# Kernel optimization log

Hardware: AMD Instinct MI355X
Metric: run time of the kernel (lower is better)

The kernel has to match this reference:

```python
import jax, jax.numpy as jnp
import numpy as np

G, P, PO, TAU = 4, 32, 128, 2.0  # n_groups, spatial_points, out_points=P*out_multiplier, level-softmax temperature
STRIDES = (4.0, 8.0, 16.0, 32.0)
EPS = 1e-5

def _ln2(x):
    # LayerNorm over last two dims, no affine (F.layer_norm(x, x.shape[-2:]))
    mu = jnp.mean(x, axis=(-2, -1), keepdims=True)
    var = jnp.var(x, axis=(-2, -1), keepdims=True)
    return (x - mu) * jax.lax.rsqrt(var + EPS)

def _ln1(x, g, b):
    mu = jnp.mean(x, axis=-1, keepdims=True)
    var = jnp.var(x, axis=-1, keepdims=True)
    return (x - mu) * jax.lax.rsqrt(var + EPS) * g + b

def _bilinear(feat, xp, yp):
    # feat: (B,G,H,W,Ce); xp,yp: (B,N,G,P) pixel coords; grid_sample bilinear,
    # zero padding, align_corners=False semantics.
    B, Gg, H, W, Ce = feat.shape
    x0 = jnp.floor(xp); y0 = jnp.floor(yp)
    wx1 = xp - x0; wy1 = yp - y0
    b_idx = jnp.arange(B)[:, None, None, None]
    g_idx = jnp.arange(Gg)[None, None, :, None]
    def gather(xi, yi):
        valid = (xi >= 0) & (xi < W) & (yi >= 0) & (yi < H)
        xc = jnp.clip(xi, 0, W - 1).astype(jnp.int32)
        yc = jnp.clip(yi, 0, H - 1).astype(jnp.int32)
        return feat[b_idx, g_idx, yc, xc] * valid[..., None]
    v00 = gather(x0, y0); v10 = gather(x0 + 1.0, y0)
    v01 = gather(x0, y0 + 1.0); v11 = gather(x0 + 1.0, y0 + 1.0)
    wx0 = 1.0 - wx1; wy0 = 1.0 - wy1
    return (v00 * (wx0 * wy0)[..., None] + v10 * (wx1 * wy0)[..., None]
            + v01 * (wx0 * wy1)[..., None] + v11 * (wx1 * wy1)[..., None])

def _forward(queries, xyzr, feats, W_off, b_off, W_param, b_param, W_out, b_out, gamma, beta):
    B, N, D = queries.shape
    Ce = feats[0].shape[1] // G  # 64 channels per group
    # learned offsets -> sample points (make_sample_points)
    offset = (queries @ W_off + b_off).reshape(B, N, G, P, 3)
    xy = xyzr[..., :2]
    z = xyzr[..., 2]
    r = xyzr[..., 3:4]
    roi_wh = (2.0 ** xyzr[..., 2:3]) * (2.0 ** jnp.concatenate([-0.5 * r, 0.5 * r], axis=-1))  # (B,N,2)
    sample_xy = xy[:, :, None, None, :] + offset[..., :2] * roi_wh[:, :, None, None, :]  # (B,N,G,P,2)
    sample_z = z[:, :, None, None] + offset[..., 2]  # (B,N,G,P) log2 scale
    # soft level assignment across the FPN pyramid
    lvl_log = jnp.log2(jnp.asarray(STRIDES, dtype=queries.dtype))
    lw = jax.nn.softmax(-((sample_z[..., None] - lvl_log) ** 2) / TAU, axis=-1)  # (B,N,G,P,L)
    # SAMPLE4D (image mode, T=1): multi-scale group-wise bilinear gather, level-weighted sum
    sampled = jnp.zeros((B, N, G, P, Ce), queries.dtype)
    for l, feat in enumerate(feats):
        H, W = feat.shape[-2:]
        featg = feat.reshape(B, G, Ce, H, W).transpose(0, 1, 3, 4, 2)  # (B,G,H,W,Ce)
        xp = sample_xy[..., 0] / STRIDES[l] - 0.5
        yp = sample_xy[..., 1] / STRIDES[l] - 0.5
        sampled = sampled + _bilinear(featg, xp, yp) * lw[..., l, None]
    # AdaptiveMixing: per-query generated channel-mix M and point-mix S
    params = (queries @ W_param + b_param).reshape(B, N, G, -1)
    M = params[..., :Ce * Ce].reshape(B, N, G, Ce, Ce)
    S = params[..., Ce * Ce:].reshape(B, N, G, PO, P)
    h = jnp.einsum('bngpc,bngcd->bngpd', sampled, M)  # channel mixing
    h = jax.nn.relu(_ln2(h))
    h = jnp.einsum('bngqp,bngpd->bngqd', S, h)        # point mixing -> (B,N,G,PO,Ce)
    h = jax.nn.relu(_ln2(h))
    h = h.reshape(B, N, G * PO * Ce)
    q = queries + h @ W_out + b_out  # out_proj + residual
    return _ln1(q, gamma, beta)      # norm_s

def setup_inputs() -> dict:
    key = jax.random.key(0)
    ks = jax.random.split(key, 12)
    B, N, D, C = 2, 300, 256, 256
    HW = [(200, 336), (100, 168), (50, 84), (25, 42)]
    inp = {}
    inp['queries'] = jax.random.normal(ks[0], (B, N, D), jnp.float32)
    u = jax.random.uniform(ks[1], (B, N, 4), jnp.float32)
    inp['xyzr'] = jnp.stack([u[..., 0] * 1344.0, u[..., 1] * 800.0,
                             2.0 + 3.0 * u[..., 2], u[..., 3] - 0.5], axis=-1)
    for i, (H, W) in enumerate(HW):
        inp[f'feat{i}'] = jax.random.normal(ks[2 + i], (B, C, H, W), jnp.float32)
    npar = G * (64 * 64 + PO * P)  # 32768
    inp['W_off'] = jax.random.normal(ks[6], (D, G * P * 3), jnp.float32) * 0.02
    inp['b_off'] = jax.random.normal(ks[7], (G * P * 3,), jnp.float32) * 0.1
    inp['W_param'] = jax.random.normal(ks[8], (D, npar), jnp.float32) * (1.0 / np.sqrt(D))
    inp['b_param'] = jnp.zeros((npar,), jnp.float32)
    inp['W_out'] = jax.random.normal(ks[9], (G * PO * 64, D), jnp.float32) * (1.0 / np.sqrt(G * PO * 64))
    inp['b_out'] = jnp.zeros((D,), jnp.float32)
    inp['gamma'] = jnp.ones((D,), jnp.float32)
    inp['beta'] = jnp.zeros((D,), jnp.float32)
    return inp

def reference(queries, xyzr, feat0, feat1, feat2, feat3, W_off, b_off, W_param, b_param, W_out, b_out, gamma, beta):
    return _forward(queries, xyzr, (feat0, feat1, feat2, feat3),
                    W_off, b_off, W_param, b_param, W_out, b_out, gamma, beta)
```

## Files before the change

kernel.cpp:

```cpp
#include <hip/hip_runtime.h>
#include <hip/hip_bf16.h>

typedef short bf16x8 __attribute__((ext_vector_type(8)));
typedef float f32x4 __attribute__((ext_vector_type(4)));
typedef unsigned short u16x4 __attribute__((ext_vector_type(4)));

#define NQ 600
#define D 256
#define NPAR 32768
#define EPS 1e-5f
#define KSPLIT 32

#define OFF_OFFS     ((size_t)0)
#define OFF_QB       ((size_t)1048576)
#define OFF_H        ((size_t)2097152)
#define OFF_PARAMS   ((size_t)41418752)
#define OFF_KPART    ((size_t)41418752)
#define OFF_WOT      ((size_t)80740352)
#define OFF_FEATT    ((size_t)97517568)

#define PIX_PER_BG 89250

__device__ __forceinline__ void gload_lds16(const void* g, void* l) {
    __builtin_amdgcn_global_load_lds((const __attribute__((address_space(1))) unsigned int*)g,
                                     (__attribute__((address_space(3))) unsigned int*)l,
                                     16, 0, 0);
}
__device__ __forceinline__ float bf2f(unsigned short us) {
    union { unsigned u; float f; } cv; cv.u = ((unsigned)us) << 16; return cv.f;
}
__device__ __forceinline__ unsigned short f2bf(float f) {
    __hip_bfloat16 h = __float2bfloat16(f);
    return *(unsigned short*)&h;
}

__global__ __launch_bounds__(256) void k_prep(
        const float* __restrict__ f0, const float* __restrict__ f1,
        const float* __restrict__ f2, const float* __restrict__ f3,
        const float* __restrict__ W_out, const float* __restrict__ q,
        __hip_bfloat16* __restrict__ featT,
        __hip_bfloat16* __restrict__ Wot, __hip_bfloat16* __restrict__ qb) {
    __shared__ float tile[32][33];
    int bid = blockIdx.x;
    int t = threadIdx.x;
    if (bid < 2792) {
        int bg = bid / 349, wblk = bid % 349;
        int lane = t & 63, w = t >> 6;
        int wid = wblk * 4 + w;
        const float* in; int HW, lvloff, wstart;
        if (wid < 1050)      { in = f0; HW = 67200; lvloff = 0;     wstart = 0; }
        else if (wid < 1313) { in = f1; HW = 16800; lvloff = 67200; wstart = 1050; }
        else if (wid < 1379) { in = f2; HW = 4200;  lvloff = 84000; wstart = 1313; }
        else                 { in = f3; HW = 1050;  lvloff = 88200; wstart = 1379; }
        int b = bg >> 2, g = bg & 3;
        int pix = (wid - wstart) * 64 + lane;
        bool ok = pix < HW;
        int pixc = ok ? pix : HW - 1;
        const float* base = in + (size_t)(b * 256 + g * 64) * HW + pixc;
        float v[64];
        #pragma unroll
        for (int c = 0; c < 64; c++) v[c] = base[(size_t)c * HW];
        if (ok) {
            __hip_bfloat16* ob = featT + ((size_t)bg * PIX_PER_BG + lvloff + pixc) * 64;
            #pragma unroll
            for (int s8 = 0; s8 < 8; s8++) {
                unsigned short o[8];
                #pragma unroll
                for (int i = 0; i < 8; i++) o[i] = f2bf(v[s8 * 8 + i]);
                *(bf16x8*)(ob + s8 * 8) = *(bf16x8*)o;
            }
        }
        return;
    }
    int idx = bid - 2792;
    if (idx < 8192) {
        int bx = idx & 7, by = idx >> 3;
        const int R = 32768, C = 256;
        int tx = t & 31, ty = t >> 5;
        int c = bx * 32 + tx;
        #pragma unroll
        for (int i = 0; i < 4; i++) {
            int rr = by * 32 + ty + i * 8;
            tile[ty + i * 8][tx] = W_out[(size_t)rr * C + c];
        }
        __syncthreads();
        int r2 = by * 32 + tx;
        #pragma unroll
        for (int i = 0; i < 4; i++) {
            int c2 = bx * 32 + ty + i * 8;
            Wot[(size_t)c2 * R + r2] = __float2bfloat16(tile[tx][ty + i * 8]);
        }
        return;
    }
    int i = (idx - 8192) * 2048 + t * 8;
    float4 v0 = *(const float4*)(q + i);
    float4 v1 = *(const float4*)(q + i + 4);
    unsigned short o[8];
    o[0] = f2bf(v0.x); o[1] = f2bf(v0.y); o[2] = f2bf(v0.z); o[3] = f2bf(v0.w);
    o[4] = f2bf(v1.x); o[5] = f2bf(v1.y); o[6] = f2bf(v1.z); o[7] = f2bf(v1.w);
    *(bf16x8*)(qb + i) = *(bf16x8*)o;
}

__global__ __launch_bounds__(256) void k_gemm1(const __hip_bfloat16* __restrict__ A,
                              const float* __restrict__ W_off, const float* __restrict__ W_param,
                              const float* __restrict__ b_off, const float* __restrict__ b_param,
                              float* __restrict__ offs, __hip_bfloat16* __restrict__ params) {
    __shared__ __align__(16) char ldsB[32768];
    int id = blockIdx.x;
    bool isOff = id < 6;
    const float* Wsrc; const float* bias; int n0; size_t C;
    if (isOff) { Wsrc = W_off; bias = b_off; n0 = id * 64; C = 384; }
    else { Wsrc = W_param; bias = b_param; n0 = (id - 6) * 64; C = 32768; }
    int t = threadIdx.x;
    int lane = t & 63, w = t >> 6;
    int la = lane & 15, lb = lane >> 4;

    #pragma unroll
    for (int i = 0; i < 16; i++) {
        int kk = i * 16 + w * 4 + (lane >> 4);
        int j4 = (lane & 15) * 4;
        float4 v = *(const float4*)(Wsrc + (size_t)kk * C + n0 + j4);
        float vv[4] = {v.x, v.y, v.z, v.w};
        #pragma unroll
        for (int u = 0; u < 4; u++) {
            int j = j4 + u;
            int addr = j * 512 + (((kk >> 3) ^ (j & 7)) * 16) + (kk & 7) * 2;
            *(unsigned short*)(ldsB + addr) = f2bf(vv[u]);
        }
    }
    __syncthreads();

    #pragma unroll 1
    for (int mt = 0; mt < 5; mt++) {
        int m0 = mt * 128;
        bf16x8 a[2][8];
        #pragma unroll
        for (int mi = 0; mi < 2; mi++) {
            int row = m0 + w * 32 + mi * 16 + la;
            row = row < NQ ? row : NQ - 1;
            #pragma unroll
            for (int ks = 0; ks < 8; ks++)
                a[mi][ks] = *(const bf16x8*)(A + (size_t)row * 256 + ks * 32 + lb * 8);
        }
        f32x4 acc[2][4];
        #pragma unroll
        for (int i = 0; i < 2; i++)
            #pragma unroll
            for (int j = 0; j < 4; j++) acc[i][j] = (f32x4)(0.f);
        #pragma unroll
        for (int ks = 0; ks < 8; ks++) {
            bf16x8 b[4];
            #pragma unroll
            for (int ni = 0; ni < 4; ni++) {
                int row = ni * 16 + la;
                int c16s = (ks * 4 + lb) ^ (row & 7);
                b[ni] = *(const bf16x8*)(ldsB + row * 512 + c16s * 16);
            }
            #pragma unroll
            for (int mi = 0; mi < 2; mi++)
                #pragma unroll
                for (int ni = 0; ni < 4; ni++)
                    acc[mi][ni] = __builtin_amdgcn_mfma_f32_16x16x32_bf16(a[mi][ks], b[ni], acc[mi][ni], 0, 0, 0);
        }
        #pragma unroll
        for (int mi = 0; mi < 2; mi++) {
            int rbase = m0 + w * 32 + mi * 16 + lb * 4;
            #pragma unroll
            for (int ni = 0; ni < 4; ni++) {
                int col = n0 + ni * 16 + la;
                float bv = bias[col];
                #pragma unroll
                for (int rg = 0; rg < 4; rg++) {
                    int row = rbase + rg;
                    if (row < NQ) {
                        if (isOff) offs[(size_t)row * 384 + col] = acc[mi][ni][rg] + bv;
                        else params[(size_t)row * NPAR + col] = __float2bfloat16(acc[mi][ni][rg] + bv);
                    }
                }
            }
        }
    }
}

#define MIX_SMP 0
#define MIX_MT  4096
#define MIX_SS  12288
#define MIX_H1T 20480
__device__ inline float2 blk_reduce2(float s, float ss, float* red, float norm) {
    __syncthreads();
    #pragma unroll
    for (int off = 32; off; off >>= 1) { s += __shfl_down(s, off); ss += __shfl_down(ss, off); }
    int wave = threadIdx.x >> 6, lane = threadIdx.x & 63;
    if (lane == 0) { red[wave * 2] = s; red[wave * 2 + 1] = ss; }
    __syncthreads();
    if (threadIdx.x == 0) {
        float a = 0.f, b = 0.f;
        #pragma unroll
        for (int i = 0; i < 4; i++) { a += red[2 * i]; b += red[2 * i + 1]; }
        red[8] = a * norm; red[9] = b * norm;
    }
    __syncthreads();
    return make_float2(red[8], red[9]);
}

__global__ __launch_bounds__(256) void k_sample_mix(const float* __restrict__ offs,
                      const float* __restrict__ xyzr,
                      const __hip_bfloat16* __restrict__ featT,
                      const __hip_bfloat16* __restrict__ params,
                      __hip_bfloat16* __restrict__ h) {
    __shared__ __align__(16) char lds[24576];
    __shared__ float smeta[32][8];
    __shared__ float red[16];
    int bid = blockIdx.x;
    int m = bid >> 2, g = bid & 3;
    int b = m / 300;
    int t = threadIdx.x;
    int lane = t & 63, w = t >> 6;
    int la = lane & 15, lb = lane >> 4;
    const __hip_bfloat16* pbase = params + (size_t)m * NPAR + g * 8192;

    #pragma unroll
    for (int r = 0; r < 2; r++) {
        int i = t + r * 256;
        int c = i >> 3, d0 = (i & 7) * 8;
        bf16x8 v = *(const bf16x8*)(pbase + i * 8);
        #pragma unroll
        for (int j = 0; j < 8; j++) {
            int d = d0 + j;
            int addr = MIX_MT + d * 128 + ((c >> 3) ^ (d & 7)) * 16 + (c & 7) * 2;
            *(unsigned short*)(lds + addr) = ((unsigned short*)&v)[j];
        }
    }
    #pragma unroll
    for (int r = 0; r < 2; r++) {
        int i = t + r * 256;
        int qr = i >> 2, c16 = i & 3;
        bf16x8 v = *(const bf16x8*)(pbase + 4096 + i * 8);
        *(bf16x8*)(lds + MIX_SS + qr * 64 + (c16 ^ (qr & 3)) * 16) = v;
    }
    if (t < 32) {
        int p = t;
        const float* op = offs + (size_t)m * 384 + (g * 32 + p) * 3;
        float o0 = op[0], o1 = op[1], o2 = op[2];
        float cx = xyzr[m * 4 + 0], cy = xyzr[m * 4 + 1], z = xyzr[m * 4 + 2], rr = xyzr[m * 4 + 3];
        smeta[p][0] = cx + o0 * exp2f(z - 0.5f * rr);
        smeta[p][1] = cy + o1 * exp2f(z + 0.5f * rr);
        float sz = z + o2;
        float e[4], mx = -1e30f;
        #pragma unroll
        for (int l = 0; l < 4; l++) { float d = sz - (float)(2 + l); e[l] = -0.5f * d * d; mx = fmaxf(mx, e[l]); }
        float ssum = 0.f;
        #pragma unroll
        for (int l = 0; l < 4; l++) { e[l] = __expf(e[l] - mx); ssum += e[l]; }
        float inv = 1.f / ssum;
        #pragma unroll
        for (int l = 0; l < 4; l++) smeta[p][2 + l] = e[l] * inv;
    }
    __syncthreads();

    int corner = lane >> 4;
    int dx = corner & 1, dy = corner >> 1;
    int ch = (lane & 15) * 4;
    const int Hs[4] = {200, 100, 50, 25};
    const int Ws[4] = {336, 168, 84, 42};
    const int Ls[4] = {0, 67200, 84000, 88200};
    const float invS[4] = {0.25f, 0.125f, 0.0625f, 0.03125f};
    const __hip_bfloat16* base_bg = featT + (size_t)(b * 4 + g) * PIX_PER_BG * 64;
    for (int pi = 0; pi < 8; pi++) {
        int p = w * 8 + pi;
        float sx = smeta[p][0], sy = smeta[p][1];
        float acc0 = 0.f, acc1 = 0.f, acc2 = 0.f, acc3 = 0.f;
        #pragma unroll
        for (int l = 0; l < 4; l++) {
            float wl = smeta[p][2 + l];
            if (wl < 1e-6f) continue;
            const int H = Hs[l], W = Ws[l];
            float xp = sx * invS[l] - 0.5f, yp = sy * invS[l] - 0.5f;
            float x0f = floorf(xp), y0f = floorf(yp);
            float wx1 = xp - x0f, wy1 = yp - y0f;
            int xi = (int)x0f + dx, yi = (int)y0f + dy;
            bool valid = (xi >= 0) && (xi < W) && (yi >= 0) && (yi < H);
            int xc = xi < 0 ? 0 : (xi >= W ? W - 1 : xi);
            int yc = yi < 0 ? 0 : (yi >= H ? H - 1 : yi);
            float cw = (dx ? wx1 : 1.f - wx1) * (dy ? wy1 : 1.f - wy1) * wl;
            if (!valid) cw = 0.f;
            const __hip_bfloat16* src = base_bg + ((size_t)Ls[l] + (size_t)yc * W + xc) * 64 + ch;
            u16x4 v = *(const u16x4*)src;
            acc0 += cw * bf2f(v[0]);
            acc1 += cw * bf2f(v[1]);
            acc2 += cw * bf2f(v[2]);
            acc3 += cw * bf2f(v[3]);
        }
        acc0 += __shfl_xor(acc0, 16); acc1 += __shfl_xor(acc1, 16);
        acc2 += __shfl_xor(acc2, 16); acc3 += __shfl_xor(acc3, 16);
        acc0 += __shfl_xor(acc0, 32); acc1 += __shfl_xor(acc1, 32);
        acc2 += __shfl_xor(acc2, 32); acc3 += __shfl_xor(acc3, 32);
        if (lane < 16) {
            unsigned short o[4];
            o[0] = f2bf(acc0); o[1] = f2bf(acc1); o[2] = f2bf(acc2); o[3] = f2bf(acc3);
            int slot = lane >> 1, half = lane & 1;
            *(u16x4*)(lds + MIX_SMP + p * 128 + ((slot ^ (p & 7)) * 16) + half * 8) = *(u16x4*)o;
        }
    }
    __syncthreads();

    f32x4 acc1v[2];
    acc1v[0] = (f32x4)(0.f); acc1v[1] = (f32x4)(0.f);
    int dcol = w * 16 + la;
    #pragma unroll
    for (int ks = 0; ks < 2; ks++) {
        bf16x8 bfr = *(const bf16x8*)(lds + MIX_MT + dcol * 128 + (((ks * 4 + lb)) ^ (dcol & 7)) * 16);
        #pragma unroll
        for (int mi = 0; mi < 2; mi++) {
            int prow = mi * 16 + la;
            bf16x8 afr = *(const bf16x8*)(lds + MIX_SMP + prow * 128 + ((ks * 4 + lb) ^ (prow & 7)) * 16);
            acc1v[mi] = __builtin_amdgcn_mfma_f32_16x16x32_bf16(afr, bfr, acc1v[mi], 0, 0, 0);
        }
    }
    float s = 0.f, ss = 0.f;
    #pragma unroll
    for (int mi = 0; mi < 2; mi++)
        #pragma unroll
        for (int j = 0; j < 4; j++) { float v = acc1v[mi][j]; s += v; ss += v * v; }
    float2 r1 = blk_reduce2(s, ss, red, 1.f / 2048.f);
    float mu = r1.x, inv = rsqrtf(r1.y - r1.x * r1.x + EPS);
    #pragma unroll
    for (int mi = 0; mi < 2; mi++) {
        u16x4 pk;
        #pragma unroll
        for (int rg = 0; rg < 4; rg++) {
            float v = (acc1v[mi][rg] - mu) * inv;
            pk[rg] = f2bf(v > 0.f ? v : 0.f);
        }
        int c16 = mi * 2 + (lb >> 1);
        int off8 = 8 * (lb & 1);
        *(u16x4*)(lds + MIX_H1T + dcol * 64 + ((c16 ^ (dcol & 3)) * 16) + off8) = pk;
    }
    __syncthreads();

    f32x4 acc2v[8];
    bf16x8 bfr2 = *(const bf16x8*)(lds + MIX_H1T + dcol * 64 + ((lb ^ (dcol & 3)) * 16));
    #pragma unroll
    for (int nj = 0; nj < 8; nj++) {
        int qrow = nj * 16 + la;
        bf16x8 afr = *(const bf16x8*)(lds + MIX_SS + qrow * 64 + ((lb ^ (qrow & 3)) * 16));
        acc2v[nj] = __builtin_amdgcn_mfma_f32_16x16x32_bf16(afr, bfr2, (f32x4)(0.f), 0, 0, 0);
    }
    s = 0.f; ss = 0.f;
    #pragma unroll
    for (int nj = 0; nj < 8; nj++)
        #pragma unroll
        for (int j = 0; j < 4; j++) { float v = acc2v[nj][j]; s += v; ss += v * v; }
    float2 r2 = blk_reduce2(s, ss, red, 1.f / 8192.f);
    float mu2 = r2.x, inv2 = rsqrtf(r2.y - r2.x * r2.x + EPS);
    __hip_bfloat16* hb = h + (size_t)m * NPAR + g * 8192;
    #pragma unroll
    for (int nj = 0; nj < 8; nj++) {
        #pragma unroll
        for (int rg = 0; rg < 4; rg++) {
            int qr = nj * 16 + lb * 4 + rg;
            float v = (acc2v[nj][rg] - mu2) * inv2;
            v = v > 0.f ? v : 0.f;
            hb[qr * 64 + dcol] = __float2bfloat16(v);
        }
    }
}

__global__ __launch_bounds__(256) void k_gemm_out(const __hip_bfloat16* __restrict__ A,
                           const __hip_bfloat16* __restrict__ Bt, float* __restrict__ kpart) {
    __shared__ __align__(16) char lds[49152];
    int bid = blockIdx.x;
    int work = (bid & 7) * 80 + (bid >> 3);
    int mblk = work % 10;
    int nz = work / 10;
    int n0 = (nz & 1) * 128;
    int z = nz >> 1;
    int m0 = mblk * 64;
    size_t k0 = (size_t)z * 1024;
    int t = threadIdx.x, lane = t & 63, w = t >> 6;
    int la = lane & 15, lb = lane >> 4;
    int wm = w >> 1, wn = w & 1;

    const char* Ag = (const char*)A;
    const char* Bg = (const char*)Bt;

    auto stage = [&](int buf, int st) {
        size_t kk = k0 + (size_t)st * 64;
        char* dstA = lds + buf * 24576;
        char* dstB = dstA + 8192;
        #pragma unroll
        for (int r = 0; r < 2; r++) {
            int p = (r * 4 + w) * 64 + lane;
            int row = p >> 3, c16 = p & 7;
            int c16s = c16 ^ (row & 7);
            int grow = m0 + row; grow = grow < NQ ? grow : NQ - 1;
            gload_lds16(Ag + ((size_t)grow * NPAR + kk) * 2 + c16s * 16, dstA + p * 16);
        }
        #pragma unroll
        for (int r = 0; r < 4; r++) {
            int p = (r * 4 + w) * 64 + lane;
            int row = p >> 3, c16 = p & 7;
            int c16s = c16 ^ (row & 7);
            gload_lds16(Bg + ((size_t)(n0 + row) * NPAR + kk) * 2 + c16s * 16, dstB + p * 16);
        }
    };

    f32x4 acc[2][4];
    #pragma unroll
    for (int i = 0; i < 2; i++)
        #pragma unroll
        for (int j = 0; j < 4; j++) acc[i][j] = (f32x4)(0.f);

    stage(0, 0);
    __syncthreads();
    for (int st = 0; st < 16; st++) {
        int buf = st & 1;
        if (st < 15) stage(buf ^ 1, st + 1);
        const char* tA = lds + buf * 24576;
        const char* tB = tA + 8192;
        #pragma unroll
        for (int ks = 0; ks < 2; ks++) {
            bf16x8 a[2], b[4];
            #pragma unroll
            for (int mi = 0; mi < 2; mi++) {
                int row = wm * 32 + mi * 16 + la;
                int c16s = (ks * 4 + lb) ^ (row & 7);
                a[mi] = *(const bf16x8*)(tA + row * 128 + c16s * 16);
            }
            #pragma unroll
            for (int ni = 0; ni < 4; ni++) {
                int row = wn * 64 + ni * 16 + la;
                int c16s = (ks * 4 + lb) ^ (row & 7);
                b[ni] = *(const bf16x8*)(tB + row * 128 + c16s * 16);
            }
            #pragma unroll
            for (int mi = 0; mi < 2; mi++)
                #pragma unroll
                for (int ni = 0; ni < 4; ni++)
                    acc[mi][ni] = __builtin_amdgcn_mfma_f32_16x16x32_bf16(a[mi], b[ni], acc[mi][ni], 0, 0, 0);
        }
        __syncthreads();
    }

    float* outp = kpart + (size_t)z * (NQ * D);
    #pragma unroll
    for (int mi = 0; mi < 2; mi++) {
        int rbase = m0 + wm * 32 + mi * 16 + lb * 4;
        #pragma unroll
        for (int ni = 0; ni < 4; ni++) {
            int col = n0 + wn * 64 + ni * 16 + la;
            #pragma unroll
            for (int rg = 0; rg < 4; rg++) {
                int row = rbase + rg;
                if (row < NQ) outp[(size_t)row * D + col] = acc[mi][ni][rg];
            }
        }
    }
}

__global__ void k_ln_out(const float* __restrict__ kpart, const float* __restrict__ queries,
                         const float* __restrict__ b_out, const float* __restrict__ gamma,
                         const float* __restrict__ beta, float* __restrict__ out) {
    int m = blockIdx.x, t = threadIdx.x;
    float x = queries[m * 256 + t] + b_out[t];
    for (int kc = 0; kc < KSPLIT; kc++) x += kpart[(size_t)kc * (NQ * D) + m * 256 + t];
    __shared__ float red[16];
    float s = x, ss = x * x;
    #pragma unroll
    for (int off = 32; off; off >>= 1) { s += __shfl_down(s, off); ss += __shfl_down(ss, off); }
    int wave = t >> 6, lane = t & 63;
    if (lane == 0) { red[wave * 2] = s; red[wave * 2 + 1] = ss; }
    __syncthreads();
    if (t == 0) {
        float a = 0.f, b = 0.f;
        #pragma unroll
        for (int i = 0; i < 4; i++) { a += red[2 * i]; b += red[2 * i + 1]; }
        red[8] = a * (1.f / 256.f); red[9] = b * (1.f / 256.f);
    }
    __syncthreads();
    float mu = red[8], var = red[9] - mu * mu;
    float inv = rsqrtf(var + EPS);
    out[m * 256 + t] = (x - mu) * inv * gamma[t] + beta[t];
}

extern "C" void kernel_launch(void* const* d_in, const int* in_sizes, int n_in,
                              void* d_out, int out_size, void* d_ws, size_t ws_size,
                              hipStream_t stream) {
    const float* queries = (const float*)d_in[0];
    const float* xyzr    = (const float*)d_in[1];
    const float* f0      = (const float*)d_in[2];
    const float* f1      = (const float*)d_in[3];
    const float* f2      = (const float*)d_in[4];
    const float* f3      = (const float*)d_in[5];
    const float* W_off   = (const float*)d_in[6];
    const float* b_off   = (const float*)d_in[7];
    const float* W_param = (const float*)d_in[8];
    const float* b_param = (const float*)d_in[9];
    const float* W_out   = (const float*)d_in[10];
    const float* b_out   = (const float*)d_in[11];
    const float* gamma   = (const float*)d_in[12];
    const float* beta    = (const float*)d_in[13];
    float* out = (float*)d_out;
    char* ws = (char*)d_ws;

    float* offs            = (float*)(ws + OFF_OFFS);
    __hip_bfloat16* qb     = (__hip_bfloat16*)(ws + OFF_QB);
    __hip_bfloat16* hbuf   = (__hip_bfloat16*)(ws + OFF_H);
    __hip_bfloat16* params = (__hip_bfloat16*)(ws + OFF_PARAMS);
    float* kpart           = (float*)(ws + OFF_KPART);
    __hip_bfloat16* Wot    = (__hip_bfloat16*)(ws + OFF_WOT);
    __hip_bfloat16* featT  = (__hip_bfloat16*)(ws + OFF_FEATT);

    k_prep<<<11059, 256, 0, stream>>>(f0, f1, f2, f3, W_out, queries, featT, Wot, qb);
    k_gemm1<<<518, 256, 0, stream>>>(qb, W_off, W_param, b_off, b_param, offs, params);
    k_sample_mix<<<2400, 256, 0, stream>>>(offs, xyzr, featT, params, hbuf);
    k_gemm_out<<<640, 256, 0, stream>>>(hbuf, Wot, kpart);
    k_ln_out<<<600, 256, 0, stream>>>(kpart, queries, b_out, gamma, beta, out);
}
```

Baseline: 189.5 us.

## Merge query-projection GEMM into prep kernel and convert queries inline

Folds the first GEMM (offsets and dynamic parameters) into the prep kernel as its leading block range, so it runs alongside the feature transpose and the W_out transpose instead of in a separate launch. Queries are now converted from fp32 to bf16 inside the GEMM loop, which removes the separate bf16 copy of the queries. The feature transpose now has each wave handle four 64-pixel groups, which cuts its block count. This saves a launch and a dependency boundary, at the cost of redundant fp32 query loads per k-step, a 32KB LDS allocation for every block type, and possible load imbalance between the branches.

```diff
diff --git a/kernel.cpp b/kernel.cpp
--- a/kernel.cpp
+++ b/kernel.cpp
@@ -12,7 +12,6 @@
 #define KSPLIT 32
 
 #define OFF_OFFS     ((size_t)0)
-#define OFF_QB       ((size_t)1048576)
 #define OFF_H        ((size_t)2097152)
 #define OFF_PARAMS   ((size_t)41418752)
 #define OFF_KPART    ((size_t)41418752)
@@ -37,148 +36,148 @@
 __global__ __launch_bounds__(256) void k_prep(
         const float* __restrict__ f0, const float* __restrict__ f1,
         const float* __restrict__ f2, const float* __restrict__ f3,
-        const float* __restrict__ W_out, const float* __restrict__ q,
-        __hip_bfloat16* __restrict__ featT,
-        __hip_bfloat16* __restrict__ Wot, __hip_bfloat16* __restrict__ qb) {
-    __shared__ float tile[32][33];
+        const float* __restrict__ W_out, const float* __restrict__ queries,
+        const float* __restrict__ W_off, const float* __restrict__ W_param,
+        const float* __restrict__ b_off, const float* __restrict__ b_param,
+        __hip_bfloat16* __restrict__ featT, __hip_bfloat16* __restrict__ Wot,
+        float* __restrict__ offs, __hip_bfloat16* __restrict__ params) {
+    __shared__ __align__(16) char smem[32768];
     int bid = blockIdx.x;
     int t = threadIdx.x;
-    if (bid < 2792) {
-        int bg = bid / 349, wblk = bid % 349;
-        int lane = t & 63, w = t >> 6;
-        int wid = wblk * 4 + w;
-        const float* in; int HW, lvloff, wstart;
-        if (wid < 1050)      { in = f0; HW = 67200; lvloff = 0;     wstart = 0; }
-        else if (wid < 1313) { in = f1; HW = 16800; lvloff = 67200; wstart = 1050; }
-        else if (wid < 1379) { in = f2; HW = 4200;  lvloff = 84000; wstart = 1313; }
-        else                 { in = f3; HW = 1050;  lvloff = 88200; wstart = 1379; }
-        int b = bg >> 2, g = bg & 3;
-        int pix = (wid - wstart) * 64 + lane;
-        bool ok = pix < HW;
-        int pixc = ok ? pix : HW - 1;
-        const float* base = in + (size_t)(b * 256 + g * 64) * HW + pixc;
-        float v[64];
-        #pragma unroll
-        for (int c = 0; c < 64; c++) v[c] = base[(size_t)c * HW];
-        if (ok) {
-            __hip_bfloat16* ob = featT + ((size_t)bg * PIX_PER_BG + lvloff + pixc) * 64;
-            #pragma unroll
-            for (int s8 = 0; s8 < 8; s8++) {
-                unsigned short o[8];
-                #pragma unroll
-                for (int i = 0; i < 8; i++) o[i] = f2bf(v[s8 * 8 + i]);
-                *(bf16x8*)(ob + s8 * 8) = *(bf16x8*)o;
-            }
-        }
-        return;
-    }
-    int idx = bid - 2792;
-    if (idx < 8192) {
-        int bx = idx & 7, by = idx >> 3;
-        const int R = 32768, C = 256;
-        int tx = t & 31, ty = t >> 5;
-        int c = bx * 32 + tx;
-        #pragma unroll
-        for (int i = 0; i < 4; i++) {
-            int rr = by * 32 + ty + i * 8;
-            tile[ty + i * 8][tx] = W_out[(size_t)rr * C + c];
+    int lane = t & 63, w = t >> 6;
+
+    if (bid < 518) {
+        bool isOff = bid < 6;
+        const float* Wsrc; const float* bias; int n0; size_t C;
+        if (isOff) { Wsrc = W_off; bias = b_off; n0 = bid * 64; C = 384; }
+        else { Wsrc = W_param; bias = b_param; n0 = (bid - 6) * 64; C = 32768; }
+        int la = lane & 15, lb = lane >> 4;
+        char* ldsB = smem;
+        #pragma unroll
+        for (int i = 0; i < 16; i++) {
+            int kk = i * 16 + w * 4 + (lane >> 4);
+            int j4 = (lane & 15) * 4;
+            float4 v = *(const float4*)(Wsrc + (size_t)kk * C + n0 + j4);
+            float vv[4] = {v.x, v.y, v.z, v.w};
+            #pragma unroll
+            for (int u = 0; u < 4; u++) {
+                int j = j4 + u;
+                int addr = j * 512 + (((kk >> 3) ^ (j & 7)) * 16) + (kk & 7) * 2;
+                *(unsigned short*)(ldsB + addr) = f2bf(vv[u]);
+            }
         }
         __syncthreads();
-        int r2 = by * 32 + tx;
-        #pragma unroll
-        for (int i = 0; i < 4; i++) {
-            int c2 = bx * 32 + ty + i * 8;
-            Wot[(size_t)c2 * R + r2] = __float2bfloat16(tile[tx][ty + i * 8]);
-        }
-        return;
-    }
-    int i = (idx - 8192) * 2048 + t * 8;
-    float4 v0 = *(const float4*)(q + i);
-    float4 v1 = *(const float4*)(q + i + 4);
-    unsigned short o[8];
-    o[0] = f2bf(v0.x); o[1] = f2bf(v0.y); o[2] = f2bf(v0.z); o[3] = f2bf(v0.w);
-    o[4] = f2bf(v1.x); o[5] = f2bf(v1.y); o[6] = f2bf(v1.z); o[7] = f2bf(v1.w);
-    *(bf16x8*)(qb + i) = *(bf16x8*)o;
-}
-
-__global__ __launch_bounds__(256) void k_gemm1(const __hip_bfloat16* __restrict__ A,
-                              const float* __restrict__ W_off, const float* __restrict__ W_param,
-                              const float* __restrict__ b_off, const float* __restrict__ b_param,
-                              float* __restrict__ offs, __hip_bfloat16* __restrict__ params) {
-    __shared__ __align__(16) char ldsB[32768];
-    int id = blockIdx.x;
-    bool isOff = id < 6;
-    const float* Wsrc; const float* bias; int n0; size_t C;
-    if (isOff) { Wsrc = W_off; bias = b_off; n0 = id * 64; C = 384; }
-    else { Wsrc = W_param; bias = b_param; n0 = (id - 6) * 64; C = 32768; }
-    int t = threadIdx.x;
-    int lane = t & 63, w = t >> 6;
-    int la = lane & 15, lb = lane >> 4;
-
-    #pragma unroll
-    for (int i = 0; i < 16; i++) {
-        int kk = i * 16 + w * 4 + (lane >> 4);
-        int j4 = (lane & 15) * 4;
-        float4 v = *(const float4*)(Wsrc + (size_t)kk * C + n0 + j4);
-        float vv[4] = {v.x, v.y, v.z, v.w};
-        #pragma unroll
-        for (int u = 0; u < 4; u++) {
-            int j = j4 + u;
-            int addr = j * 512 + (((kk >> 3) ^ (j & 7)) * 16) + (kk & 7) * 2;
-            *(unsigned short*)(ldsB + addr) = f2bf(vv[u]);
-        }
-    }
-    __syncthreads();
-
-    #pragma unroll 1
-    for (int mt = 0; mt < 5; mt++) {
-        int m0 = mt * 128;
-        bf16x8 a[2][8];
-        #pragma unroll
-        for (int mi = 0; mi < 2; mi++) {
-            int row = m0 + w * 32 + mi * 16 + la;
-            row = row < NQ ? row : NQ - 1;
-            #pragma unroll
-            for (int ks = 0; ks < 8; ks++)
-                a[mi][ks] = *(const bf16x8*)(A + (size_t)row * 256 + ks * 32 + lb * 8);
-        }
-        f32x4 acc[2][4];
-        #pragma unroll
-        for (int i = 0; i < 2; i++)
-            #pragma unroll
-            for (int j = 0; j < 4; j++) acc[i][j] = (f32x4)(0.f);
-        #pragma unroll
-        for (int ks = 0; ks < 8; ks++) {
-            bf16x8 b[4];
-            #pragma unroll
-            for (int ni = 0; ni < 4; ni++) {
-                int row = ni * 16 + la;
-                int c16s = (ks * 4 + lb) ^ (row & 7);
-                b[ni] = *(const bf16x8*)(ldsB + row * 512 + c16s * 16);
-            }
-            #pragma unroll
-            for (int mi = 0; mi < 2; mi++)
-                #pragma unroll
-                for (int ni = 0; ni < 4; ni++)
-                    acc[mi][ni] = __builtin_amdgcn_mfma_f32_16x16x32_bf16(a[mi][ks], b[ni], acc[mi][ni], 0, 0, 0);
-        }
-        #pragma unroll
-        for (int mi = 0; mi < 2; mi++) {
-            int rbase = m0 + w * 32 + mi * 16 + lb * 4;
-            #pragma unroll
-            for (int ni = 0; ni < 4; ni++) {
-                int col = n0 + ni * 16 + la;
-                float bv = bias[col];
-                #pragma unroll
-                for (int rg = 0; rg < 4; rg++) {
-                    int row = rbase + rg;
-                    if (row < NQ) {
-                        if (isOff) offs[(size_t)row * 384 + col] = acc[mi][ni][rg] + bv;
-                        else params[(size_t)row * NPAR + col] = __float2bfloat16(acc[mi][ni][rg] + bv);
+        #pragma unroll 1
+        for (int mt = 0; mt < 5; mt++) {
+            int m0 = mt * 128;
+            int arow[2];
+            #pragma unroll
+            for (int mi = 0; mi < 2; mi++) {
+                int row = m0 + w * 32 + mi * 16 + la;
+                arow[mi] = row < NQ ? row : NQ - 1;
+            }
+            f32x4 acc[2][4];
+            #pragma unroll
+            for (int i = 0; i < 2; i++)
+                #pragma unroll
+                for (int j = 0; j < 4; j++) acc[i][j] = (f32x4)(0.f);
+            #pragma unroll
+            for (int ks = 0; ks < 8; ks++) {
+                bf16x8 a2[2], b[4];
+                #pragma unroll
+                for (int mi = 0; mi < 2; mi++) {
+                    const float* qr = queries + (size_t)arow[mi] * 256 + ks * 32 + lb * 8;
+                    float4 v0 = *(const float4*)qr;
+                    float4 v1 = *(const float4*)(qr + 4);
+                    unsigned short o[8];
+                    o[0] = f2bf(v0.x); o[1] = f2bf(v0.y); o[2] = f2bf(v0.z); o[3] = f2bf(v0.w);
+                    o[4] = f2bf(v1.x); o[5] = f2bf(v1.y); o[6] = f2bf(v1.z); o[7] = f2bf(v1.w);
+                    a2[mi] = *(bf16x8*)o;
+                }
+                #pragma unroll
+                for (int ni = 0; ni < 4; ni++) {
+                    int row = ni * 16 + la;
+                    int c16s = (ks * 4 + lb) ^ (row & 7);
+                    b[ni] = *(const bf16x8*)(ldsB + row * 512 + c16s * 16);
+                }
+                #pragma unroll
+                for (int mi = 0; mi < 2; mi++)
+                    #pragma unroll
+                    for (int ni = 0; ni < 4; ni++)
+                        acc[mi][ni] = __builtin_amdgcn_mfma_f32_16x16x32_bf16(a2[mi], b[ni], acc[mi][ni], 0, 0, 0);
+            }
+            #pragma unroll
+            for (int mi = 0; mi < 2; mi++) {
+                int rbase = m0 + w * 32 + mi * 16 + lb * 4;
+                #pragma unroll
+                for (int ni = 0; ni < 4; ni++) {
+                    int col = n0 + ni * 16 + la;
+                    float bv = bias[col];
+                    #pragma unroll
+                    for (int rg = 0; rg < 4; rg++) {
+                        int row = rbase + rg;
+                        if (row < NQ) {
+                            if (isOff) offs[(size_t)row * 384 + col] = acc[mi][ni][rg] + bv;
+                            else params[(size_t)row * NPAR + col] = __float2bfloat16(acc[mi][ni][rg] + bv);
+                        }
                     }
                 }
             }
         }
+        return;
+    }
+    if (bid < 1222) {
+        int fid = bid - 518;
+        int bg = fid / 88, wblk = fid % 88;
+        int wid = wblk * 4 + w;
+        if (wid >= 351) return;
+        const float* in; int HW, lvloff, wstart;
+        if (wid < 263)      { in = f0; HW = 67200; lvloff = 0;     wstart = 0; }
+        else if (wid < 329) { in = f1; HW = 16800; lvloff = 67200; wstart = 263; }
+        else if (wid < 346) { in = f2; HW = 4200;  lvloff = 84000; wstart = 329; }
+        else                { in = f3; HW = 1050;  lvloff = 88200; wstart = 346; }
+        int b = bg >> 2, g = bg & 3;
+        const float* plane = in + (size_t)(b * 256 + g * 64) * HW;
+        int pix0 = (wid - wstart) * 256 + lane;
+        #pragma unroll 1
+        for (int g4 = 0; g4 < 4; g4++) {
+            int pix = pix0 + g4 * 64;
+            bool ok = pix < HW;
+            int pixc = ok ? pix : HW - 1;
+            const float* base = plane + pixc;
+            float v[64];
+            #pragma unroll
+            for (int c = 0; c < 64; c++) v[c] = base[(size_t)c * HW];
+            if (ok) {
+                __hip_bfloat16* ob = featT + ((size_t)bg * PIX_PER_BG + lvloff + pixc) * 64;
+                #pragma unroll
+                for (int s8 = 0; s8 < 8; s8++) {
+                    unsigned short o[8];
+                    #pragma unroll
+                    for (int i = 0; i < 8; i++) o[i] = f2bf(v[s8 * 8 + i]);
+                    *(bf16x8*)(ob + s8 * 8) = *(bf16x8*)o;
+                }
+            }
+        }
+        return;
+    }
+    int idx = bid - 1222;
+    float (*tile)[33] = (float(*)[33])smem;
+    int bx = idx & 7, by = idx >> 3;
+    const int R = 32768, C = 256;
+    int tx = t & 31, ty = t >> 5;
+    int c = bx * 32 + tx;
+    #pragma unroll
+    for (int i = 0; i < 4; i++) {
+        int rr = by * 32 + ty + i * 8;
+        tile[ty + i * 8][tx] = W_out[(size_t)rr * C + c];
+    }
+    __syncthreads();
+    int r2 = by * 32 + tx;
+    #pragma unroll
+    for (int i = 0; i < 4; i++) {
+        int c2 = bx * 32 + ty + i * 8;
+        Wot[(size_t)c2 * R + r2] = __float2bfloat16(tile[tx][ty + i * 8]);
     }
 }
 
@@ -504,15 +503,14 @@
     char* ws = (char*)d_ws;
 
     float* offs            = (float*)(ws + OFF_OFFS);
-    __hip_bfloat16* qb     = (__hip_bfloat16*)(ws + OFF_QB);
     __hip_bfloat16* hbuf   = (__hip_bfloat16*)(ws + OFF_H);
     __hip_bfloat16* params = (__hip_bfloat16*)(ws + OFF_PARAMS);
     float* kpart           = (float*)(ws + OFF_KPART);
     __hip_bfloat16* Wot    = (__hip_bfloat16*)(ws + OFF_WOT);
     __hip_bfloat16* featT  = (__hip_bfloat16*)(ws + OFF_FEATT);
 
-    k_prep<<<11059, 256, 0, stream>>>(f0, f1, f2, f3, W_out, queries, featT, Wot, qb);
-    k_gemm1<<<518, 256, 0, stream>>>(qb, W_off, W_param, b_off, b_param, offs, params);
+    k_prep<<<9414, 256, 0, stream>>>(f0, f1, f2, f3, W_out, queries, W_off, W_param,
+                                     b_off, b_param, featT, Wot, offs, params);
     k_sample_mix<<<2400, 256, 0, stream>>>(offs, xyzr, featT, params, hbuf);
     k_gemm_out<<<640, 256, 0, stream>>>(hbuf, Wot, kpart);
     k_ln_out<<<600, 256, 0, stream>>>(kpart, queries, b_out, gamma, beta, out);
```

After: 244.4 us. 1.29x slower.
